# Optimization experiments

Hardware: AMD Instinct MI355X
Metric: run time of the kernel (lower is better)

Reference implementation:

```python
import jax, jax.numpy as jnp
import numpy as np

M = 5            # Anderson history size
LAM = 1e-4       # Tikhonov regularization on the Gram matrix
MAX_ITER = 50
TOL = 1e-5
BETA = 1.0
ALPHA = 0.9      # damping


def anderson(f, x0, m=M, lam=LAM, max_iter=MAX_ITER, tol=TOL, beta=BETA):
    """Anderson acceleration for fixed-point iteration (faithful to torch ref).

    x0: [bsz, L]. Variable history size n=min(k,m) is handled by masking the
    (m+1)x(m+1) system: inactive slots get an identity row -> alpha_j = 0.
    """
    bsz, L = x0.shape
    dt = x0.dtype
    F0 = f(x0)
    F1 = f(F0)
    X = jnp.zeros((bsz, m, L), dt).at[:, 0].set(x0).at[:, 1].set(F0)
    Fh = jnp.zeros((bsz, m, L), dt).at[:, 0].set(F0).at[:, 1].set(F1)
    eye_m = jnp.eye(m, dtype=dt)

    def body(carry):
        k, X, Fh, _ = carry
        n = jnp.minimum(k, m)
        active = (jnp.arange(m) < n).astype(dt)          # [m]
        G = Fh - X                                        # inactive rows are zero
        Hc = jnp.einsum('bil,bjl->bij', G, G) + lam * eye_m
        m2 = active[:, None] * active[None, :]
        # zero out inactive rows/cols, put 1 on their diagonal (=> alpha_j = 0)
        Hc = Hc * m2 + eye_m * (1.0 - active)
        H = jnp.zeros((bsz, m + 1, m + 1), dt)
        H = H.at[:, 0, 1:].set(active).at[:, 1:, 0].set(active).at[:, 1:, 1:].set(Hc)
        y = jnp.zeros((bsz, m + 1, 1), dt).at[:, 0, 0].set(1.0)
        alpha_c = jnp.linalg.solve(H, y)[:, 1:, 0]        # [bsz, m]
        xnew = beta * jnp.einsum('bm,bml->bl', alpha_c, Fh) \
             + (1.0 - beta) * jnp.einsum('bm,bml->bl', alpha_c, X)
        slot = k % m
        X = X.at[:, slot].set(xnew)
        fnew = f(xnew)
        Fh = Fh.at[:, slot].set(fnew)
        res = jnp.linalg.norm(fnew - xnew) / (1e-5 + jnp.linalg.norm(fnew))
        return (k + 1, X, Fh, res)

    def cond(carry):
        k, _, _, res = carry
        return jnp.logical_and(k < max_iter, res >= tol)

    k, X, Fh, res = jax.lax.while_loop(
        cond, body, (jnp.array(2), X, Fh, jnp.array(np.inf, dt)))
    return X[:, (k - 1) % m]


def make_f(x, maskf, W, b, alpha):
    """Damped forward step: z -> softmax_ch((1-a)z + a*Conv(mask-inject(z)))."""
    bsz, C, H, Wd = x.shape

    def f(zflat):
        z = zflat.reshape(bsz, C, H, Wd)
        zm = z * (1.0 - maskf) + maskf * x               # inject observed parts
        lin = jax.lax.conv_general_dilated(
            zm, W, window_strides=(1, 1), padding='SAME',
            dimension_numbers=('NCHW', 'OIHW', 'NCHW')) + b[None, :, None, None]
        pre = (1.0 - alpha) * z + alpha * lin
        return jax.nn.softmax(pre, axis=1).reshape(bsz, -1)

    return f


def setup_inputs() -> dict:
    key = jax.random.key(0)
    k1, k2, k3 = jax.random.split(key, 3)
    bsz, C, H, Wd = 32, 128, 32, 32
    x = jax.random.normal(k1, (bsz, C, H, Wd), jnp.float32)
    mask = jax.random.randint(k2, (bsz, 1, H, Wd), 0, 2).astype(jnp.int32)
    W = jax.random.normal(k3, (C, C, 3, 3), jnp.float32) * 0.05  # keep map contractive
    b = jnp.zeros((C,), jnp.float32)
    return {"x": x, "W": W, "b": b, "mask": mask}


def reference(x, W, b, mask):
    bsz, C, H, Wd = x.shape
    maskf = mask.astype(x.dtype)
    f = make_f(x, maskf, W, b, ALPHA)
    # z_start = softmax(zeros) over channel dim -> uniform 1/C
    z0 = jnp.full((bsz, C * H * Wd), 1.0 / C, x.dtype)
    zstar = anderson(f, z0)
    zn = f(zstar)            # one extra step, as in the torch forward
    return zn                # [bsz, C*H*W]
```

## Files before the change

### kernel.cpp

```cpp
#include <hip/hip_runtime.h>


typedef unsigned short u16;
using short8 = __attribute__((ext_vector_type(8))) short;
using f32x4  = __attribute__((ext_vector_type(4))) float;

#define SLOT 4194304

struct Ctrl { int done; int last_slot; };

__device__ __forceinline__ u16 f2bf(float f) {
  unsigned u = __builtin_bit_cast(unsigned, f);
  unsigned r = (u + 0x7FFFu + ((u >> 16) & 1u)) >> 16;
  return (u16)r;
}
__device__ __forceinline__ float bf2f(u16 h) {
  unsigned u = ((unsigned)h) << 16;
  return __builtin_bit_cast(float, u);
}

__global__ void __launch_bounds__(256) k_prepw(const float* __restrict__ W,
    u16* __restrict__ Wb, Ctrl* ctrl) {
  if (blockIdx.x == 0 && threadIdx.x == 0) { ctrl->done = 0; ctrl->last_slot = 4; }
  int t = blockIdx.x * 256 + threadIdx.x;
  int o = t >> 14;
  int rem = t & 16383;
  int cout = rem >> 7, cin = rem & 127;
  float v = W[(size_t)cout * 1152 + (size_t)cin * 9 + o];
  Wb[(size_t)o * 16384 + (size_t)cout * 128 + cin] = f2bf(v);
}

__global__ void __launch_bounds__(256) k_prepx(const float* __restrict__ x,
    const int* __restrict__ mask_, u16* __restrict__ xsw) {
  int t = blockIdx.x * 256 + threadIdx.x;
  int g = t >> 15, p = t & 32767;
  int nb = p >> 10, gp = p & 1023, px = p & 31;
  short8 xv;
#pragma unroll
  for (int u = 0; u < 8; ++u) {
    float v = x[(size_t)nb * 131072 + (size_t)(g * 8 + u) * 1024 + gp];
    xv[u] = (short)f2bf(v);
  }
  (void)mask_;
  *(short8*)(xsw + (size_t)p * 128 + (size_t)((g ^ (px & 7)) << 3)) = xv;
}

__global__ void __launch_bounds__(1024) k_iter(
    const int e,
    const u16* __restrict__ xsw, const int* __restrict__ mask_,
    const u16* __restrict__ Wb, const float* __restrict__ bias,
    float* __restrict__ Fh, u16* __restrict__ G_all,
    float* __restrict__ gram, float* __restrict__ gpart,
    float* __restrict__ resp, Ctrl* __restrict__ ctrl)
{
  __shared__ char smem[129344];
  char*  As       = smem;
  float* zbuf     = (float*)(smem + 52224);
  float* rowmax_s = (float*)(smem + 119808);
  float* rowsum_s = (float*)(smem + 123904);
  float* red      = (float*)(smem + 128000);
  float* alpha_s  = (float*)(smem + 128512);
  float* res_s    = (float*)(smem + 128544);
  int*   mk6      = (int*)(smem + 128560);

  if (ctrl->done) return;

  const int tid = threadIdx.x;
  const int wid = tid >> 6, lane = tid & 63;
  const int lhi = lane >> 4, llo = lane & 15;
  const int wr = wid >> 3, wc = wid & 7;
  const int bid = blockIdx.x;
  const int n = bid >> 3, y0 = (bid & 7) << 2;
  const int pixbase = (n << 10) + (y0 << 5);
  const int colc = (wc << 4) + llo;
  const int slot = e % 5;
  const int nact = e < 5 ? e : 5;

  if (e >= 3) {
    if (tid < 64) {
      float sd = 0.f, sf = 0.f;
      for (int i = tid; i < 256; i += 64) { sd += resp[2 * i]; sf += resp[2 * i + 1]; }
#pragma unroll
      for (int off = 1; off < 64; off <<= 1) { sd += __shfl_xor(sd, off); sf += __shfl_xor(sf, off); }
      if (tid == 0) res_s[0] = sqrtf(sd) / (1e-5f + sqrtf(sf));
    }
    __syncthreads();
    if (res_s[0] < 1e-5f) {
      if (tid == 0) { ctrl->done = 1; ctrl->last_slot = (e - 1) % 5; }
      return;
    }
  }

  if (tid < 192) {
    int gy = y0 - 1 + (tid >> 5);
    mk6[tid] = ((unsigned)gy < 32u) ? mask_[(n << 10) + (gy << 5) + (tid & 31)] : 0;
  }
  if (e >= 1 && tid >= 960 && tid < 965) {
    int j = tid - 960;
    float s = 0.f;
#pragma unroll
    for (int c = 0; c < 8; ++c) s += gpart[(size_t)((n << 3) + c) * 5 + j];
    int sp = (e - 1) % 5;
    gram[n * 25 + sp * 5 + j] = s;
    gram[n * 25 + j * 5 + sp] = s;
  }
  __syncthreads();
  if (e >= 2) {
    if (tid == 0) {
      float A[6][7];
      for (int i = 0; i < 5; ++i)
        for (int j = 0; j < 5; ++j)
          A[i + 1][j + 1] = (i < nact && j < nact)
              ? gram[n * 25 + i * 5 + j] + ((i == j) ? 1e-4f : 0.f)
              : ((i == j) ? 1.f : 0.f);
      A[0][0] = 0.f;
      for (int j = 0; j < 5; ++j) { float aj = (j < nact) ? 1.f : 0.f; A[0][j + 1] = aj; A[j + 1][0] = aj; }
      A[0][6] = 1.f;
      for (int i = 1; i < 6; ++i) A[i][6] = 0.f;
      for (int c = 0; c < 6; ++c) {
        int p = c; float mx = fabsf(A[c][c]);
        for (int r = c + 1; r < 6; ++r) { float v = fabsf(A[r][c]); if (v > mx) { mx = v; p = r; } }
        if (p != c) for (int q = c; q < 7; ++q) { float tmp = A[c][q]; A[c][q] = A[p][q]; A[p][q] = tmp; }
        float piv = A[c][c];
        for (int r = c + 1; r < 6; ++r) {
          float fr = A[r][c] / piv;
          for (int q = c; q < 7; ++q) A[r][q] -= fr * A[c][q];
        }
      }
      float sol[6];
      for (int r = 5; r >= 0; --r) {
        float s = A[r][6];
        for (int q = r + 1; q < 6; ++q) s -= A[r][q] * sol[q];
        sol[r] = s / A[r][r];
      }
      for (int j = 0; j < 5; ++j) alpha_s[j] = sol[j + 1];
    }
  } else if (tid < 5) {
    alpha_s[tid] = (tid == 0) ? 1.f : 0.f;
  }
  __syncthreads();

  {
    const float a0 = alpha_s[0], a1 = alpha_s[1], a2 = alpha_s[2],
                a3 = alpha_s[3], a4 = alpha_s[4];
#pragma unroll
    for (int uu = 0; uu < 3; ++uu) {
      int unit = (uu << 10) + tid;
      int grp = unit & 15, px6 = unit >> 4;
      int row6 = px6 >> 5, px = px6 & 31;
      int gy = y0 - 1 + row6;
      char* dst = As + row6 * 8704 + ((px + 1) << 8) + ((grp ^ (px & 7)) << 4);
      short8 w = {0, 0, 0, 0, 0, 0, 0, 0};
      if ((unsigned)gy < 32u) {
        int gpix = (n << 10) + (gy << 5) + px;
        f32x4 va, vb;
        if (e == 0) {
          const f32x4 cz = {0.0078125f, 0.0078125f, 0.0078125f, 0.0078125f};
          va = cz; vb = cz;
        } else {
          const float* fb = Fh + (size_t)gpix * 128 + (grp << 3);
          va = a0 * *(const f32x4*)fb;
          vb = a0 * *(const f32x4*)(fb + 4);
          if (nact > 1) { va += a1 * *(const f32x4*)(fb + SLOT);     vb += a1 * *(const f32x4*)(fb + SLOT + 4); }
          if (nact > 2) { va += a2 * *(const f32x4*)(fb + 2 * SLOT); vb += a2 * *(const f32x4*)(fb + 2 * SLOT + 4); }
          if (nact > 3) { va += a3 * *(const f32x4*)(fb + 3 * SLOT); vb += a3 * *(const f32x4*)(fb + 3 * SLOT + 4); }
          if (nact > 4) { va += a4 * *(const f32x4*)(fb + 4 * SLOT); vb += a4 * *(const f32x4*)(fb + 4 * SLOT + 4); }
        }
        if (mk6[px6]) {
          w = *(const short8*)(xsw + (size_t)gpix * 128 + ((grp ^ (px & 7)) << 3));
        } else {
#pragma unroll
          for (int i = 0; i < 4; ++i) { w[i] = (short)f2bf(va[i]); w[4 + i] = (short)f2bf(vb[i]); }
        }
        if (row6 >= 1 && row6 <= 4) {
          float* zb = zbuf + (px6 - 32) * 132 + (grp << 3);
          *(f32x4*)zb = va;
          *(f32x4*)(zb + 4) = vb;
        }
      }
      *(short8*)dst = w;
    }
    if (tid < 192) {
      int r = tid >> 5, cc = tid & 31;
      int col = (cc < 16) ? 0 : 33, gc = cc & 15;
      f32x4 zz = {0.f, 0.f, 0.f, 0.f};
      *(f32x4*)(As + r * 8704 + (col << 8) + (gc << 4)) = zz;
    }
  }
  __syncthreads();

  f32x4 acc[4];
  {
    const f32x4 z4 = {0.f, 0.f, 0.f, 0.f};
    acc[0] = z4; acc[1] = z4; acc[2] = z4; acc[3] = z4;
  }
#pragma unroll
  for (int o = 0; o < 9; ++o) {
    const int dy = o / 3, dx = o % 3;
    short8 bfr[4];
#pragma unroll
    for (int kk = 0; kk < 4; ++kk)
      bfr[kk] = *(const short8*)(Wb + o * 16384 + colc * 128 + ((kk << 2) + lhi) * 8);
#pragma unroll
    for (int kk = 0; kk < 4; ++kk) {
      const int kg = (kk << 2) + lhi;
#pragma unroll
      for (int m2 = 0; m2 < 4; ++m2) {
        int p = (wr << 6) + (m2 << 4) + llo;
        int r = (p >> 5) + dy, cl = (p & 31) + dx;
        int sg = kg ^ ((cl - 1) & 7);
        short8 af = *(const short8*)(As + r * 8704 + (cl << 8) + (sg << 4));
        acc[m2] = __builtin_amdgcn_mfma_f32_16x16x32_bf16(af, bfr[kk], acc[m2], 0, 0, 0);
      }
    }
  }

  const float bc = bias[colc];
  float zr[16];
#pragma unroll
  for (int m2 = 0; m2 < 4; ++m2)
#pragma unroll
    for (int rr = 0; rr < 4; ++rr) {
      int p = (wr << 6) + (m2 << 4) + (lhi << 2) + rr;
      float z = zbuf[p * 132 + colc];
      zr[m2 * 4 + rr] = z;
      acc[m2][rr] = 0.1f * z + 0.9f * (acc[m2][rr] + bc);
    }
#pragma unroll
  for (int m2 = 0; m2 < 4; ++m2)
#pragma unroll
    for (int rr = 0; rr < 4; ++rr) {
      float v = acc[m2][rr];
      v = fmaxf(v, __shfl_xor(v, 1)); v = fmaxf(v, __shfl_xor(v, 2));
      v = fmaxf(v, __shfl_xor(v, 4)); v = fmaxf(v, __shfl_xor(v, 8));
      if (llo == 0) rowmax_s[((wr << 6) + (m2 << 4) + (lhi << 2) + rr) * 8 + wc] = v;
    }
  __syncthreads();
#pragma unroll
  for (int m2 = 0; m2 < 4; ++m2)
#pragma unroll
    for (int rr = 0; rr < 4; ++rr) {
      int p = (wr << 6) + (m2 << 4) + (lhi << 2) + rr;
      f32x4 m0 = *(const f32x4*)&rowmax_s[p * 8];
      f32x4 m1 = *(const f32x4*)&rowmax_s[p * 8 + 4];
      float M = fmaxf(fmaxf(fmaxf(m0[0], m0[1]), fmaxf(m0[2], m0[3])),
                      fmaxf(fmaxf(m1[0], m1[1]), fmaxf(m1[2], m1[3])));
      float ev = __expf(acc[m2][rr] - M);
      acc[m2][rr] = ev;
      float s = ev;
      s += __shfl_xor(s, 1); s += __shfl_xor(s, 2);
      s += __shfl_xor(s, 4); s += __shfl_xor(s, 8);
      if (llo == 0) rowsum_s[p * 8 + wc] = s;
    }
  __syncthreads();

  float sd = 0.f, sf = 0.f;
  float gd16[16];
#pragma unroll
  for (int m2 = 0; m2 < 4; ++m2)
#pragma unroll
    for (int rr = 0; rr < 4; ++rr) {
      int p = (wr << 6) + (m2 << 4) + (lhi << 2) + rr;
      f32x4 s0 = *(const f32x4*)&rowsum_s[p * 8];
      f32x4 s1 = *(const f32x4*)&rowsum_s[p * 8 + 4];
      float S = s0[0] + s0[1] + s0[2] + s0[3] + s1[0] + s1[1] + s1[2] + s1[3];
      float fnew = acc[m2][rr] * (1.0f / S);
      Fh[(size_t)slot * SLOT + (size_t)(pixbase + p) * 128 + colc] = fnew;
      float gd = fnew - zr[m2 * 4 + rr];
      gd16[m2 * 4 + rr] = gd;
      sd += gd * gd; sf += fnew * fnew;
    }
  {
    short8 h0, h1;
#pragma unroll
    for (int i = 0; i < 8; ++i) { h0[i] = (short)f2bf(gd16[i]); h1[i] = (short)f2bf(gd16[8 + i]); }
    size_t gb = (size_t)bid * 16384 + (size_t)tid * 16;
    u16* Gs = G_all + (size_t)slot * SLOT;
    *(short8*)(Gs + gb) = h0;
    *(short8*)(Gs + gb + 8) = h1;
    const int jmax = e < 4 ? e : 4;
    float gacc[5];
#pragma unroll
    for (int j = 0; j < 5; ++j) {
      if (j > jmax) { gacc[j] = 0.f; continue; }
      if (j == slot) {
        float a = 0.f;
#pragma unroll
        for (int i = 0; i < 16; ++i) a += gd16[i] * gd16[i];
        gacc[j] = a;
      } else {
        short8 q0 = *(const short8*)(G_all + (size_t)j * SLOT + gb);
        short8 q1 = *(const short8*)(G_all + (size_t)j * SLOT + gb + 8);
        float a = 0.f;
#pragma unroll
        for (int i = 0; i < 8; ++i)
          a += gd16[i] * bf2f((u16)q0[i]) + gd16[8 + i] * bf2f((u16)q1[i]);
        gacc[j] = a;
      }
    }
    float vals[7] = {gacc[0], gacc[1], gacc[2], gacc[3], gacc[4], sd, sf};
#pragma unroll
    for (int i = 0; i < 7; ++i) {
      float v = vals[i];
#pragma unroll
      for (int off = 1; off < 64; off <<= 1) v += __shfl_xor(v, off);
      if (lane == 0) red[wid * 8 + i] = v;
    }
  }
  __syncthreads();
  if (tid < 7) {
    float s = 0.f;
#pragma unroll
    for (int w = 0; w < 16; ++w) s += red[w * 8 + tid];
    if (tid < 5)       gpart[(size_t)bid * 5 + tid] = s;
    else if (tid == 5) resp[bid * 2] = s;
    else               resp[bid * 2 + 1] = s;
  }
}

__global__ void __launch_bounds__(256) k_out(const float* __restrict__ Fh,
    const Ctrl* __restrict__ ctrl, float* __restrict__ out)
{
  __shared__ float T[64][129];
  int slot = ctrl->last_slot;
  const float* src = Fh + (size_t)slot * SLOT;
  int bid = blockIdx.x;
  int nb = bid >> 4, seg = bid & 15;
  int pixbase = (nb << 10) + (seg << 6);
  for (int it = 0; it < 32; ++it) {
    int idx = it * 256 + threadIdx.x;
    int pix = idx >> 7, c = idx & 127;
    T[pix][c] = src[(size_t)(pixbase + pix) * 128 + c];
  }
  __syncthreads();
  for (int it = 0; it < 32; ++it) {
    int idx = it * 256 + threadIdx.x;
    int c = idx >> 6, pix = idx & 63;
    out[(size_t)((nb << 7) + c) * 1024 + (seg << 6) + pix] = T[pix][c];
  }
}

extern "C" void kernel_launch(void* const* d_in, const int* in_sizes, int n_in,
                              void* d_out, int out_size, void* d_ws, size_t ws_size,
                              hipStream_t stream) {
  const float* x    = (const float*)d_in[0];
  const float* W    = (const float*)d_in[1];
  const float* bias = (const float*)d_in[2];
  const int*   mask = (const int*)d_in[3];
  float* out = (float*)d_out;
  char* ws = (char*)d_ws;

  float* Fh    = (float*)(ws + 0);
  u16*   G     = (u16*)(ws + 83886080);
  u16*   xsw   = (u16*)(ws + 125829120);
  u16*   Wb    = (u16*)(ws + 134217728);
  float* gram  = (float*)(ws + 134512640);
  float* gpart = (float*)(ws + 134515840);
  float* resp  = (float*)(ws + 134520960);
  Ctrl*  ctrl  = (Ctrl*)(ws + 134523008);

  k_prepw<<<576, 256, 0, stream>>>(W, Wb, ctrl);
  k_prepx<<<2048, 256, 0, stream>>>(x, mask, xsw);
  for (int e = 0; e < 50; ++e)
    k_iter<<<256, 1024, 0, stream>>>(e, xsw, mask, Wb, bias,
                                     Fh, G, gram, gpart, resp, ctrl);
  k_out<<<512, 256, 0, stream>>>(Fh, ctrl, out);
  (void)in_sizes; (void)n_in; (void)out_size; (void)ws_size;
}
```

Measured before the change: 415.5 us.

## Store Anderson history in per-thread fragment layout and halve block tiles

The iteration kernel now covers two image rows per block with 512 threads instead of four rows with 1024, and shared memory drops from about 129KB to about 40KB so more blocks can be resident per CU. The history buffers Fh and G are stored in a per-thread MFMA-fragment order, so each thread reads its own mixed input and writes its outputs as contiguous vectors, and the fp32 z staging buffer in shared memory goes away. Halo rows are reconstructed from the permuted layout with strided scalar gathers, the block index is swizzled across XCDs, and the output kernel is rewritten to transpose from the new layout. The cost is extra index arithmetic, uncoalesced halo loads, and more halo recomputation relative to the smaller tiles.

```diff
diff --git a/kernel.cpp b/kernel.cpp
--- a/kernel.cpp
+++ b/kernel.cpp
@@ -31,7 +31,7 @@
 }
 
 __global__ void __launch_bounds__(256) k_prepx(const float* __restrict__ x,
-    const int* __restrict__ mask_, u16* __restrict__ xsw) {
+    u16* __restrict__ xsw) {
   int t = blockIdx.x * 256 + threadIdx.x;
   int g = t >> 15, p = t & 32767;
   int nb = p >> 10, gp = p & 1023, px = p & 31;
@@ -41,45 +41,44 @@
     float v = x[(size_t)nb * 131072 + (size_t)(g * 8 + u) * 1024 + gp];
     xv[u] = (short)f2bf(v);
   }
-  (void)mask_;
   *(short8*)(xsw + (size_t)p * 128 + (size_t)((g ^ (px & 7)) << 3)) = xv;
 }
 
-__global__ void __launch_bounds__(1024) k_iter(
+__global__ void __launch_bounds__(512, 8) k_iter(
     const int e,
     const u16* __restrict__ xsw, const int* __restrict__ mask_,
     const u16* __restrict__ Wb, const float* __restrict__ bias,
-    float* __restrict__ Fh, u16* __restrict__ G_all,
+    float* __restrict__ Fhp, u16* __restrict__ Gp,
     float* __restrict__ gram, float* __restrict__ gpart,
     float* __restrict__ resp, Ctrl* __restrict__ ctrl)
 {
-  __shared__ char smem[129344];
+  __shared__ char smem[39552];
   char*  As       = smem;
-  float* zbuf     = (float*)(smem + 52224);
-  float* rowmax_s = (float*)(smem + 119808);
-  float* rowsum_s = (float*)(smem + 123904);
-  float* red      = (float*)(smem + 128000);
-  float* alpha_s  = (float*)(smem + 128512);
-  float* res_s    = (float*)(smem + 128544);
-  int*   mk6      = (int*)(smem + 128560);
+  float* rowmax_s = (float*)(smem + 34816);
+  float* rowsum_s = (float*)(smem + 36864);
+  float* red      = (float*)(smem + 38912);
+  float* alpha_s  = (float*)(smem + 39168);
+  float* res_s    = (float*)(smem + 39188);
+  int*   mk_s     = (int*)(smem + 39296);
 
   if (ctrl->done) return;
 
   const int tid = threadIdx.x;
-  const int wid = tid >> 6, lane = tid & 63;
+  const int wc = tid >> 6, lane = tid & 63;
   const int lhi = lane >> 4, llo = lane & 15;
-  const int wr = wid >> 3, wc = wid & 7;
-  const int bid = blockIdx.x;
-  const int n = bid >> 3, y0 = (bid & 7) << 2;
-  const int pixbase = (n << 10) + (y0 << 5);
+  const int bhw = blockIdx.x;
+  const int lbid = ((bhw & 7) << 6) + (bhw >> 3);
+  const int n = lbid >> 4, y0 = (lbid & 15) << 1;
+  const int gpix0 = (n << 10) + (y0 << 5);
   const int colc = (wc << 4) + llo;
   const int slot = e % 5;
   const int nact = e < 5 ? e : 5;
+  const size_t base = ((size_t)lbid * 512 + tid) * 16;
 
   if (e >= 3) {
     if (tid < 64) {
       float sd = 0.f, sf = 0.f;
-      for (int i = tid; i < 256; i += 64) { sd += resp[2 * i]; sf += resp[2 * i + 1]; }
+      for (int i = tid; i < 512; i += 64) { sd += resp[2 * i]; sf += resp[2 * i + 1]; }
 #pragma unroll
       for (int off = 1; off < 64; off <<= 1) { sd += __shfl_xor(sd, off); sf += __shfl_xor(sf, off); }
       if (tid == 0) res_s[0] = sqrtf(sd) / (1e-5f + sqrtf(sf));
@@ -91,15 +90,12 @@
     }
   }
 
-  if (tid < 192) {
-    int gy = y0 - 1 + (tid >> 5);
-    mk6[tid] = ((unsigned)gy < 32u) ? mask_[(n << 10) + (gy << 5) + (tid & 31)] : 0;
-  }
-  if (e >= 1 && tid >= 960 && tid < 965) {
-    int j = tid - 960;
+  if (tid < 64) mk_s[tid] = mask_[gpix0 + tid];
+  if (e >= 1 && tid >= 64 && tid < 69) {
+    int j = tid - 64;
     float s = 0.f;
 #pragma unroll
-    for (int c = 0; c < 8; ++c) s += gpart[(size_t)((n << 3) + c) * 5 + j];
+    for (int c = 0; c < 16; ++c) s += gpart[(size_t)((n << 4) + c) * 5 + j];
     int sp = (e - 1) % 5;
     gram[n * 25 + sp * 5 + j] = s;
     gram[n * 25 + j * 5 + sp] = s;
@@ -140,52 +136,91 @@
   }
   __syncthreads();
 
-  {
-    const float a0 = alpha_s[0], a1 = alpha_s[1], a2 = alpha_s[2],
-                a3 = alpha_s[3], a4 = alpha_s[4];
-#pragma unroll
-    for (int uu = 0; uu < 3; ++uu) {
-      int unit = (uu << 10) + tid;
-      int grp = unit & 15, px6 = unit >> 4;
-      int row6 = px6 >> 5, px = px6 & 31;
-      int gy = y0 - 1 + row6;
-      char* dst = As + row6 * 8704 + ((px + 1) << 8) + ((grp ^ (px & 7)) << 4);
-      short8 w = {0, 0, 0, 0, 0, 0, 0, 0};
-      if ((unsigned)gy < 32u) {
-        int gpix = (n << 10) + (gy << 5) + px;
-        f32x4 va, vb;
-        if (e == 0) {
-          const f32x4 cz = {0.0078125f, 0.0078125f, 0.0078125f, 0.0078125f};
-          va = cz; vb = cz;
-        } else {
-          const float* fb = Fh + (size_t)gpix * 128 + (grp << 3);
-          va = a0 * *(const f32x4*)fb;
-          vb = a0 * *(const f32x4*)(fb + 4);
-          if (nact > 1) { va += a1 * *(const f32x4*)(fb + SLOT);     vb += a1 * *(const f32x4*)(fb + SLOT + 4); }
-          if (nact > 2) { va += a2 * *(const f32x4*)(fb + 2 * SLOT); vb += a2 * *(const f32x4*)(fb + 2 * SLOT + 4); }
-          if (nact > 3) { va += a3 * *(const f32x4*)(fb + 3 * SLOT); vb += a3 * *(const f32x4*)(fb + 3 * SLOT + 4); }
-          if (nact > 4) { va += a4 * *(const f32x4*)(fb + 4 * SLOT); vb += a4 * *(const f32x4*)(fb + 4 * SLOT + 4); }
-        }
-        if (mk6[px6]) {
-          w = *(const short8*)(xsw + (size_t)gpix * 128 + ((grp ^ (px & 7)) << 3));
-        } else {
-#pragma unroll
-          for (int i = 0; i < 4; ++i) { w[i] = (short)f2bf(va[i]); w[4 + i] = (short)f2bf(vb[i]); }
-        }
-        if (row6 >= 1 && row6 <= 4) {
-          float* zb = zbuf + (px6 - 32) * 132 + (grp << 3);
-          *(f32x4*)zb = va;
-          *(f32x4*)(zb + 4) = vb;
+  float a0 = 1.f, a1 = 0.f, a2 = 0.f, a3 = 0.f, a4 = 0.f;
+  if (e >= 1) { a0 = alpha_s[0]; a1 = alpha_s[1]; a2 = alpha_s[2]; a3 = alpha_s[3]; a4 = alpha_s[4]; }
+
+  f32x4 zv[4];
+  if (e == 0) {
+    const f32x4 cz = {0.0078125f, 0.0078125f, 0.0078125f, 0.0078125f};
+    zv[0] = cz; zv[1] = cz; zv[2] = cz; zv[3] = cz;
+  } else {
+    const float* fb = Fhp + base;
+#pragma unroll
+    for (int q = 0; q < 4; ++q) zv[q] = a0 * *(const f32x4*)(fb + q * 4);
+    if (nact > 1) {
+#pragma unroll
+      for (int q = 0; q < 4; ++q) zv[q] += a1 * *(const f32x4*)(fb + SLOT + q * 4);
+    }
+    if (nact > 2) {
+#pragma unroll
+      for (int q = 0; q < 4; ++q) zv[q] += a2 * *(const f32x4*)(fb + 2 * SLOT + q * 4);
+    }
+    if (nact > 3) {
+#pragma unroll
+      for (int q = 0; q < 4; ++q) zv[q] += a3 * *(const f32x4*)(fb + 3 * SLOT + q * 4);
+    }
+    if (nact > 4) {
+#pragma unroll
+      for (int q = 0; q < 4; ++q) zv[q] += a4 * *(const f32x4*)(fb + 4 * SLOT + q * 4);
+    }
+  }
+
+#pragma unroll
+  for (int m2 = 0; m2 < 4; ++m2)
+#pragma unroll
+    for (int rr = 0; rr < 4; ++rr) {
+      int p = (m2 << 4) + (lhi << 2) + rr;
+      int px = p & 31, row = 1 + (p >> 5);
+      int sg = (colc >> 3) ^ (px & 7);
+      u16 w;
+      if (mk_s[p])
+        w = xsw[(size_t)(gpix0 + p) * 128 + (sg << 3) + (colc & 7)];
+      else
+        w = f2bf(zv[m2][rr]);
+      *(u16*)(As + row * 8704 + ((px + 1) << 8) + (sg << 4) + ((colc & 7) << 1)) = w;
+    }
+
+#pragma unroll
+  for (int uu = 0; uu < 2; ++uu) {
+    int u = (uu << 9) + tid;
+    int rsel = u >> 9;
+    int row = rsel * 3;
+    int gy = y0 - 1 + row;
+    int idx = u & 511;
+    int px = idx >> 4, grp = idx & 15;
+    char* dst = As + row * 8704 + ((px + 1) << 8) + ((grp ^ (px & 7)) << 4);
+    short8 w = {0, 0, 0, 0, 0, 0, 0, 0};
+    if ((unsigned)gy < 32u) {
+      int gpix = (n << 10) + (gy << 5) + px;
+      if (mask_[gpix]) {
+        w = *(const short8*)(xsw + (size_t)gpix * 128 + ((grp ^ (px & 7)) << 3));
+      } else if (e == 0) {
+#pragma unroll
+        for (int i = 0; i < 8; ++i) w[i] = (short)0x3C00;
+      } else {
+        int bidh = (n << 4) + (gy >> 1);
+        int pl = ((gy & 1) << 5) + px;
+        int elem = ((pl >> 4) << 2) + (pl & 3);
+        int tb = ((grp >> 1) << 6) + (((pl >> 2) & 3) << 4) + ((grp & 1) << 3);
+        const float* fb2 = Fhp + ((size_t)bidh * 512 + tb) * 16 + elem;
+#pragma unroll
+        for (int i = 0; i < 8; ++i) {
+          float s = a0 * fb2[i * 16];
+          if (nact > 1) s += a1 * fb2[SLOT + i * 16];
+          if (nact > 2) s += a2 * fb2[2 * SLOT + i * 16];
+          if (nact > 3) s += a3 * fb2[3 * SLOT + i * 16];
+          if (nact > 4) s += a4 * fb2[4 * SLOT + i * 16];
+          w[i] = (short)f2bf(s);
         }
       }
-      *(short8*)dst = w;
-    }
-    if (tid < 192) {
-      int r = tid >> 5, cc = tid & 31;
-      int col = (cc < 16) ? 0 : 33, gc = cc & 15;
-      f32x4 zz = {0.f, 0.f, 0.f, 0.f};
-      *(f32x4*)(As + r * 8704 + (col << 8) + (gc << 4)) = zz;
-    }
+    }
+    *(short8*)dst = w;
+  }
+  if (tid < 128) {
+    int r = tid >> 5, cc = tid & 31;
+    int col = (cc < 16) ? 0 : 33, gc = cc & 15;
+    f32x4 zz = {0.f, 0.f, 0.f, 0.f};
+    *(f32x4*)(As + r * 8704 + (col << 8) + (gc << 4)) = zz;
   }
   __syncthreads();
 
@@ -206,7 +241,7 @@
       const int kg = (kk << 2) + lhi;
 #pragma unroll
       for (int m2 = 0; m2 < 4; ++m2) {
-        int p = (wr << 6) + (m2 << 4) + llo;
+        int p = (m2 << 4) + llo;
         int r = (p >> 5) + dy, cl = (p & 31) + dx;
         int sg = kg ^ ((cl - 1) & 7);
         short8 af = *(const short8*)(As + r * 8704 + (cl << 8) + (sg << 4));
@@ -216,16 +251,11 @@
   }
 
   const float bc = bias[colc];
-  float zr[16];
 #pragma unroll
   for (int m2 = 0; m2 < 4; ++m2)
 #pragma unroll
-    for (int rr = 0; rr < 4; ++rr) {
-      int p = (wr << 6) + (m2 << 4) + (lhi << 2) + rr;
-      float z = zbuf[p * 132 + colc];
-      zr[m2 * 4 + rr] = z;
-      acc[m2][rr] = 0.1f * z + 0.9f * (acc[m2][rr] + bc);
-    }
+    for (int rr = 0; rr < 4; ++rr)
+      acc[m2][rr] = 0.1f * zv[m2][rr] + 0.9f * (acc[m2][rr] + bc);
 #pragma unroll
   for (int m2 = 0; m2 < 4; ++m2)
 #pragma unroll
@@ -233,14 +263,14 @@
       float v = acc[m2][rr];
       v = fmaxf(v, __shfl_xor(v, 1)); v = fmaxf(v, __shfl_xor(v, 2));
       v = fmaxf(v, __shfl_xor(v, 4)); v = fmaxf(v, __shfl_xor(v, 8));
-      if (llo == 0) rowmax_s[((wr << 6) + (m2 << 4) + (lhi << 2) + rr) * 8 + wc] = v;
+      if (llo == 0) rowmax_s[((m2 << 4) + (lhi << 2) + rr) * 8 + wc] = v;
     }
   __syncthreads();
 #pragma unroll
   for (int m2 = 0; m2 < 4; ++m2)
 #pragma unroll
     for (int rr = 0; rr < 4; ++rr) {
-      int p = (wr << 6) + (m2 << 4) + (lhi << 2) + rr;
+      int p = (m2 << 4) + (lhi << 2) + rr;
       f32x4 m0 = *(const f32x4*)&rowmax_s[p * 8];
       f32x4 m1 = *(const f32x4*)&rowmax_s[p * 8 + 4];
       float M = fmaxf(fmaxf(fmaxf(m0[0], m0[1]), fmaxf(m0[2], m0[3])),
@@ -257,27 +287,29 @@
   float sd = 0.f, sf = 0.f;
   float gd16[16];
 #pragma unroll
-  for (int m2 = 0; m2 < 4; ++m2)
+  for (int m2 = 0; m2 < 4; ++m2) {
+    f32x4 fr;
 #pragma unroll
     for (int rr = 0; rr < 4; ++rr) {
-      int p = (wr << 6) + (m2 << 4) + (lhi << 2) + rr;
+      int p = (m2 << 4) + (lhi << 2) + rr;
       f32x4 s0 = *(const f32x4*)&rowsum_s[p * 8];
       f32x4 s1 = *(const f32x4*)&rowsum_s[p * 8 + 4];
       float S = s0[0] + s0[1] + s0[2] + s0[3] + s1[0] + s1[1] + s1[2] + s1[3];
       float fnew = acc[m2][rr] * (1.0f / S);
-      Fh[(size_t)slot * SLOT + (size_t)(pixbase + p) * 128 + colc] = fnew;
-      float gd = fnew - zr[m2 * 4 + rr];
+      fr[rr] = fnew;
+      float gd = fnew - zv[m2][rr];
       gd16[m2 * 4 + rr] = gd;
       sd += gd * gd; sf += fnew * fnew;
     }
+    *(f32x4*)(Fhp + (size_t)slot * SLOT + base + m2 * 4) = fr;
+  }
   {
     short8 h0, h1;
 #pragma unroll
     for (int i = 0; i < 8; ++i) { h0[i] = (short)f2bf(gd16[i]); h1[i] = (short)f2bf(gd16[8 + i]); }
-    size_t gb = (size_t)bid * 16384 + (size_t)tid * 16;
-    u16* Gs = G_all + (size_t)slot * SLOT;
-    *(short8*)(Gs + gb) = h0;
-    *(short8*)(Gs + gb + 8) = h1;
+    u16* Gs = Gp + (size_t)slot * SLOT + base;
+    *(short8*)(Gs) = h0;
+    *(short8*)(Gs + 8) = h1;
     const int jmax = e < 4 ? e : 4;
     float gacc[5];
 #pragma unroll
@@ -289,8 +321,8 @@
         for (int i = 0; i < 16; ++i) a += gd16[i] * gd16[i];
         gacc[j] = a;
       } else {
-        short8 q0 = *(const short8*)(G_all + (size_t)j * SLOT + gb);
-        short8 q1 = *(const short8*)(G_all + (size_t)j * SLOT + gb + 8);
+        short8 q0 = *(const short8*)(Gp + (size_t)j * SLOT + base);
+        short8 q1 = *(const short8*)(Gp + (size_t)j * SLOT + base + 8);
         float a = 0.f;
 #pragma unroll
         for (int i = 0; i < 8; ++i)
@@ -304,39 +336,51 @@
       float v = vals[i];
 #pragma unroll
       for (int off = 1; off < 64; off <<= 1) v += __shfl_xor(v, off);
-      if (lane == 0) red[wid * 8 + i] = v;
+      if (lane == 0) red[wc * 8 + i] = v;
     }
   }
   __syncthreads();
   if (tid < 7) {
     float s = 0.f;
 #pragma unroll
-    for (int w = 0; w < 16; ++w) s += red[w * 8 + tid];
-    if (tid < 5)       gpart[(size_t)bid * 5 + tid] = s;
-    else if (tid == 5) resp[bid * 2] = s;
-    else               resp[bid * 2 + 1] = s;
-  }
-}
-
-__global__ void __launch_bounds__(256) k_out(const float* __restrict__ Fh,
+    for (int w = 0; w < 8; ++w) s += red[w * 8 + tid];
+    if (tid < 5)       gpart[(size_t)lbid * 5 + tid] = s;
+    else if (tid == 5) resp[lbid * 2] = s;
+    else               resp[lbid * 2 + 1] = s;
+  }
+}
+
+__global__ void __launch_bounds__(512) k_out(const float* __restrict__ Fhp,
     const Ctrl* __restrict__ ctrl, float* __restrict__ out)
 {
-  __shared__ float T[64][129];
+  __shared__ float T[64 * 129];
   int slot = ctrl->last_slot;
-  const float* src = Fh + (size_t)slot * SLOT;
-  int bid = blockIdx.x;
-  int nb = bid >> 4, seg = bid & 15;
-  int pixbase = (nb << 10) + (seg << 6);
-  for (int it = 0; it < 32; ++it) {
-    int idx = it * 256 + threadIdx.x;
-    int pix = idx >> 7, c = idx & 127;
-    T[pix][c] = src[(size_t)(pixbase + pix) * 128 + c];
-  }
-  __syncthreads();
-  for (int it = 0; it < 32; ++it) {
-    int idx = it * 256 + threadIdx.x;
-    int c = idx >> 6, pix = idx & 63;
-    out[(size_t)((nb << 7) + c) * 1024 + (seg << 6) + pix] = T[pix][c];
+  const int tid = threadIdx.x;
+  const int wc = tid >> 6, lane = tid & 63;
+  const int lhi = lane >> 4, llo = lane & 15;
+  const int bhw = blockIdx.x;
+  const int lbid = ((bhw & 7) << 6) + (bhw >> 3);
+  const int n = lbid >> 4, y0 = (lbid & 15) << 1;
+  const size_t base = (size_t)slot * SLOT + ((size_t)lbid * 512 + tid) * 16;
+#pragma unroll
+  for (int m2 = 0; m2 < 4; ++m2) {
+    f32x4 v = *(const f32x4*)(Fhp + base + m2 * 4);
+#pragma unroll
+    for (int rr = 0; rr < 4; ++rr) {
+      int p = (m2 << 4) + (lhi << 2) + rr;
+      T[p * 129 + (wc << 4) + llo] = v[rr];
+    }
+  }
+  __syncthreads();
+  int c = tid >> 2, q = tid & 3;
+  int row = q >> 1, xs = (q & 1) << 4;
+  float* ob = out + (((size_t)(n << 7) + c) << 10) + ((y0 + row) << 5) + xs;
+#pragma unroll
+  for (int i2 = 0; i2 < 4; ++i2) {
+    f32x4 v;
+#pragma unroll
+    for (int i = 0; i < 4; ++i) v[i] = T[((row << 5) + xs + (i2 << 2) + i) * 129 + c];
+    *(f32x4*)(ob + (i2 << 2)) = v;
   }
 }
 
@@ -350,20 +394,20 @@
   float* out = (float*)d_out;
   char* ws = (char*)d_ws;
 
-  float* Fh    = (float*)(ws + 0);
-  u16*   G     = (u16*)(ws + 83886080);
+  float* Fhp   = (float*)(ws + 0);
+  u16*   Gp    = (u16*)(ws + 83886080);
   u16*   xsw   = (u16*)(ws + 125829120);
   u16*   Wb    = (u16*)(ws + 134217728);
   float* gram  = (float*)(ws + 134512640);
   float* gpart = (float*)(ws + 134515840);
-  float* resp  = (float*)(ws + 134520960);
-  Ctrl*  ctrl  = (Ctrl*)(ws + 134523008);
+  float* resp  = (float*)(ws + 134526080);
+  Ctrl*  ctrl  = (Ctrl*)(ws + 134530176);
 
   k_prepw<<<576, 256, 0, stream>>>(W, Wb, ctrl);
-  k_prepx<<<2048, 256, 0, stream>>>(x, mask, xsw);
+  k_prepx<<<2048, 256, 0, stream>>>(x, xsw);
   for (int e = 0; e < 50; ++e)
-    k_iter<<<256, 1024, 0, stream>>>(e, xsw, mask, Wb, bias,
-                                     Fh, G, gram, gpart, resp, ctrl);
-  k_out<<<512, 256, 0, stream>>>(Fh, ctrl, out);
+    k_iter<<<512, 512, 0, stream>>>(e, xsw, mask, Wb, bias,
+                                    Fhp, Gp, gram, gpart, resp, ctrl);
+  k_out<<<512, 512, 0, stream>>>(Fhp, ctrl, out);
   (void)in_sizes; (void)n_in; (void)out_size; (void)ws_size;
 }
```

Measured after the change: 812.5 us. 95.6% more time.
